# Performance work log

Hardware: AMD Instinct MI355X
Metric: run time of the kernel (lower is better)

The kernel has to match this reference:

```python
import jax, jax.numpy as jnp
import numpy as np

B, F, N, C = 2, 16, 128, 1280
MID = 128
CH = [320, 640, 1280, 1280]
DS = [16, 32, 64, 64]


def setup_inputs() -> dict:
    key = jax.random.key(0)
    ks = jax.random.split(key, 16)
    inp = {}
    inp["point_embedding"] = jax.random.normal(ks[0], (B, N, C), jnp.float32)
    inp["keypoints"] = jax.random.uniform(ks[1], (B, F, N, 2), dtype=jnp.float32)
    inp["subsets"] = jax.random.randint(ks[2], (B, F, N), -1, 2).astype(jnp.int32)
    inp["pose_latents"] = jax.random.normal(ks[3], (B, F, 4, 32, 32), jnp.float32)
    inp["w1s"] = jax.random.normal(ks[4], (4, C, MID), jnp.float32) * 0.02
    inp["b1s"] = jnp.zeros((4, MID), jnp.float32)
    for l, ch in enumerate(CH):
        inp[f"w2_{l}"] = jax.random.normal(ks[5 + l], (MID, ch), jnp.float32) * 0.02
        inp[f"b2_{l}"] = jnp.zeros((ch,), jnp.float32)
    inp["w"] = 512
    inp["h"] = 512
    return inp


def _nearest(x, h2, w2):
    # torch nn.Upsample(mode='nearest'): src = floor(dst * in/out)
    H, W = x.shape[-2], x.shape[-1]
    ih = (jnp.arange(h2) * H) // h2
    iw = (jnp.arange(w2) * W) // w2
    return x[:, ih][:, :, iw]


def _core(point_embedding, keypoints, subsets, w1s, b1s, w2s, b2s, w, h):
    Bb, Nn, Cc = point_embedding.shape
    Ff = keypoints.shape[1]
    H0, W0 = h // DS[0], w // DS[0]
    dt = point_embedding.dtype

    kx, ky = keypoints[..., 0], keypoints[..., 1]            # [B,F,N]
    valid = (jnp.minimum(kx, ky) >= 0) & (subsets != -1)
    px = jnp.clip(jnp.floor(kx * W0).astype(jnp.int32), 0, W0 - 1)
    py = jnp.clip(jnp.floor(ky * H0).astype(jnp.int32), 0, H0 - 1)
    bf = jnp.arange(Bb)[:, None, None] * Ff + jnp.arange(Ff)[None, :, None]
    flat = jnp.where(valid, (bf * H0 + py) * W0 + px, 0).reshape(-1)
    wts = valid.astype(dt).reshape(-1)

    # hit count per cell; level_count = max(hits, 1) matches torch's count-from-one logic
    hits = jnp.zeros(Bb * Ff * H0 * W0, dt).at[flat].add(wts)
    emb = jnp.broadcast_to(point_embedding[:, None], (Bb, Ff, Nn, Cc)).reshape(-1, Cc)
    sums = jnp.zeros((Bb * Ff * H0 * W0, Cc), dt).at[flat].add(emb * wts[:, None])
    grid = (sums / jnp.maximum(hits, 1.0)[:, None]).reshape(Bb, Ff, H0, W0, Cc)
    mask = (hits > 0).astype(dt).reshape(Bb, Ff, H0, W0)

    outs = []
    for l in range(4):
        h2, w2 = h // DS[l], w // DS[l]
        hid = jax.nn.silu(jnp.einsum('bfhwc,cm->bfhwm', grid, w1s[l]) + b1s[l])
        feat = jnp.einsum('bfhwm,mk->bfhwk', hid, w2s[l]) + b2s[l]
        feat = feat * mask[..., None]
        feat = feat.reshape(Bb * Ff, H0, W0, -1)
        if (h2, w2) != (H0, W0):
            # torch bilinear, align_corners=False (half-pixel), no antialias
            feat = jax.image.resize(feat, (Bb * Ff, h2, w2, feat.shape[-1]),
                                    method='bilinear', antialias=False)
        m = _nearest(mask.reshape(Bb * Ff, H0, W0), h2, w2)
        feat = feat * m[..., None]
        outs.append(feat.reshape(Bb, Ff, h2, w2, -1).transpose(0, 1, 4, 2, 3))
    loss_mask = jnp.ones((Bb, Ff, 4, H0, W0), dt)  # loss_type='global'
    return tuple(outs), loss_mask


def reference(point_embedding, keypoints, subsets, pose_latents, w1s, b1s,
              w2_0, b2_0, w2_1, b2_1, w2_2, b2_2, w2_3, b2_3, w, h):
    outs, loss_mask = _core(point_embedding, keypoints, subsets, w1s, b1s,
                            (w2_0, w2_1, w2_2, w2_3), (b2_0, b2_1, b2_2, b2_3), w, h)
    return (*outs, loss_mask)
```

## Files before the change

kernel.cpp:

```cpp
#include <hip/hip_runtime.h>
#include <cstdint>
#include <cstddef>

#define NPT 128
#define CC 1280
#define MID 128

typedef __attribute__((ext_vector_type(8))) short bf16x8;
typedef __attribute__((ext_vector_type(4))) float f32x4;

__device__ __forceinline__ unsigned short f2bf(float f) {
  unsigned u = __builtin_bit_cast(unsigned, f);
  u += 0x7FFFu + ((u >> 16) & 1u);
  return (unsigned short)(u >> 16);
}

struct KArgs {
  const float *w2_0, *w2_1, *w2_2, *w2_3;
  unsigned short *W2T0, *W2T1, *W2T2, *W2T3;
  const float* kp;
  const int* subsets;
  int* counts;
  int* plist;
  float* lossm;
  const float* pe;
  const float* w1s;
  const float* b1s;
  float* part;
  unsigned short* H;
  const float *b20, *b21, *b22, *b23;
  float *out0, *out1, *out2, *out3;
};

__device__ __forceinline__ void pe1_unit(const KArgs& a, int unit, int tid, char* smem) {
  unsigned short* Asl = (unsigned short*)smem;
  unsigned short* Bsl = (unsigned short*)(smem + 8192);
  int nt = unit & 7, mt = (unit >> 3) & 3, kz = unit >> 5;
  int n0 = nt * 64, m0 = mt * 64;
  int l = n0 >> 7, m0c = n0 & 127;
  const float* wbase = a.w1s + (size_t)l * CC * MID + m0c;
  int lane = tid & 63;
  int wave = tid >> 6;
  int lr = lane & 15, lk = lane >> 4;
  int choff = (wave & 1) * 32, spoff = (wave >> 1) * 32;
  f32x4 acc00 = {0.f, 0.f, 0.f, 0.f}, acc01 = acc00, acc10 = acc00, acc11 = acc00;
  for (int sub = 0; sub < 5; ++sub) {
    int kc0 = kz * 320 + sub * 64;
    __syncthreads();
    for (int u = tid; u < 512; u += 256) {
      int r = u >> 3, g = u & 7;
      const float* src = a.pe + (size_t)(m0 + r) * CC + kc0 + g * 8;
      float4 v0 = *reinterpret_cast<const float4*>(src);
      float4 v1 = *reinterpret_cast<const float4*>(src + 4);
      uint4 pk;
      pk.x = (unsigned)f2bf(v0.x) | ((unsigned)f2bf(v0.y) << 16);
      pk.y = (unsigned)f2bf(v0.z) | ((unsigned)f2bf(v0.w) << 16);
      pk.z = (unsigned)f2bf(v1.x) | ((unsigned)f2bf(v1.y) << 16);
      pk.w = (unsigned)f2bf(v1.z) | ((unsigned)f2bf(v1.w) << 16);
      *reinterpret_cast<uint4*>(&Asl[r * 64 + ((g ^ (r & 7)) << 3)]) = pk;
    }
    for (int u = tid; u < 512; u += 256) {
      int r = u & 63, gg = u >> 6;
      float vv[8];
#pragma unroll
      for (int j = 0; j < 8; ++j)
        vv[j] = wbase[(size_t)(kc0 + gg * 8 + j) * MID + r];
      uint4 pk;
      pk.x = (unsigned)f2bf(vv[0]) | ((unsigned)f2bf(vv[1]) << 16);
      pk.y = (unsigned)f2bf(vv[2]) | ((unsigned)f2bf(vv[3]) << 16);
      pk.z = (unsigned)f2bf(vv[4]) | ((unsigned)f2bf(vv[5]) << 16);
      pk.w = (unsigned)f2bf(vv[6]) | ((unsigned)f2bf(vv[7]) << 16);
      *reinterpret_cast<uint4*>(&Bsl[r * 64 + ((gg ^ (r & 7)) << 3)]) = pk;
    }
    __syncthreads();
#pragma unroll
    for (int kk = 0; kk < 64; kk += 32) {
      int gbase = (kk >> 3) + lk;
      int r0w = choff + lr, r1w = choff + 16 + lr;
      int r0a = spoff + lr, r1a = spoff + 16 + lr;
      bf16x8 wf0 = *reinterpret_cast<const bf16x8*>(&Bsl[r0w * 64 + ((gbase ^ (r0w & 7)) << 3)]);
      bf16x8 wf1 = *reinterpret_cast<const bf16x8*>(&Bsl[r1w * 64 + ((gbase ^ (r1w & 7)) << 3)]);
      bf16x8 af0 = *reinterpret_cast<const bf16x8*>(&Asl[r0a * 64 + ((gbase ^ (r0a & 7)) << 3)]);
      bf16x8 af1 = *reinterpret_cast<const bf16x8*>(&Asl[r1a * 64 + ((gbase ^ (r1a & 7)) << 3)]);
      acc00 = __builtin_amdgcn_mfma_f32_16x16x32_bf16(wf0, af0, acc00, 0, 0, 0);
      acc01 = __builtin_amdgcn_mfma_f32_16x16x32_bf16(wf0, af1, acc01, 0, 0, 0);
      acc10 = __builtin_amdgcn_mfma_f32_16x16x32_bf16(wf1, af0, acc10, 0, 0, 0);
      acc11 = __builtin_amdgcn_mfma_f32_16x16x32_bf16(wf1, af1, acc11, 0, 0, 0);
    }
  }
  float* pb = a.part + (size_t)kz * 131072;
#define PEPI(ACC, CI, SI)                                                      \
  {                                                                            \
    int spl = spoff + (SI) * 16 + lr;                                          \
    int chl = choff + (CI) * 16 + lk * 4;                                      \
    float4 v = make_float4(ACC[0], ACC[1], ACC[2], ACC[3]);                    \
    *reinterpret_cast<float4*>(&pb[(size_t)(m0 + spl) * 512 + n0 + chl]) = v;  \
  }
  PEPI(acc00, 0, 0)
  PEPI(acc01, 0, 1)
  PEPI(acc10, 1, 0)
  PEPI(acc11, 1, 1)
#undef PEPI
}

__device__ __forceinline__ void cheap_unit(const KArgs& a, int c, int tid, char* smem) {
  if (c < 32) {
    int bf = c;
    int* lcnt = (int*)smem;
    for (int i = tid; i < 1024; i += 256) lcnt[i] = 0;
    __syncthreads();
    if (tid < NPT) {
      int p = bf * NPT + tid;
      float kx = a.kp[2 * p], ky = a.kp[2 * p + 1];
      int sub = a.subsets[p];
      if (fminf(kx, ky) >= 0.f && sub != -1) {
        int px = (int)floorf(kx * 32.f);
        px = px < 0 ? 0 : (px > 31 ? 31 : px);
        int py = (int)floorf(ky * 32.f);
        py = py < 0 ? 0 : (py > 31 ? 31 : py);
        int cell = py * 32 + px;
        int slot = atomicAdd(&lcnt[cell], 1);
        if (slot < 32) a.plist[((size_t)bf * 1024 + cell) * 32 + slot] = tid;
      }
    }
    __syncthreads();
    for (int i = tid; i < 1024; i += 256) a.counts[bf * 1024 + i] = lcnt[i];
  } else if (c < 472) {
    float (*ts)[33] = (float(*)[33])smem;
    int local = c - 32;
    const float* w2;
    unsigned short* wt;
    int ch;
    if (local < 40) { w2 = a.w2_0; wt = a.W2T0; ch = 320; }
    else if (local < 120) { w2 = a.w2_1; wt = a.W2T1; ch = 640; local -= 40; }
    else if (local < 280) { w2 = a.w2_2; wt = a.W2T2; ch = 1280; local -= 120; }
    else { w2 = a.w2_3; wt = a.W2T3; ch = 1280; local -= 280; }
    int ctiles = ch >> 5;
    int mt = local / ctiles, ct = local % ctiles;
    int m0 = mt * 32, c0 = ct * 32;
    int i = tid >> 5, j = tid & 31;
#pragma unroll
    for (int r = 0; r < 4; ++r) {
      int m = r * 8 + i;
      ts[m][j] = w2[(size_t)(m0 + m) * ch + c0 + j];
    }
    __syncthreads();
#pragma unroll
    for (int r = 0; r < 4; ++r) {
      int cc = r * 8 + i;
      wt[(size_t)(c0 + cc) * 128 + m0 + j] = f2bf(ts[j][cc]);
    }
  } else {
    int idx = (c - 472) * 256 + tid;
    *reinterpret_cast<float4*>(a.lossm + (size_t)idx * 4) = make_float4(1.f, 1.f, 1.f, 1.f);
  }
}

__device__ __forceinline__ void hid_range(const KArgs& a, int base, int n, int tid,
                                          int* ccache, int* lst) {
  if (tid < n) ccache[tid] = a.counts[base + tid];
  __syncthreads();
  for (int q = 0; q < n; ++q) {
    int c = ccache[q];
    if (c == 0) continue;
    __syncthreads();
    int cell = base + q;
    int cu = c < 32 ? c : 32;
    if (tid < cu) lst[tid] = a.plist[(size_t)cell * 32 + tid];
    __syncthreads();
    int bat = cell >> 14;
    float invc = 1.f / (float)c;
    float sx = 0.f, sy = 0.f;
    for (int i = 0; i < cu; ++i) {
      const float2* rp = reinterpret_cast<const float2*>(
          a.part + (size_t)(bat * NPT + lst[i]) * 512);
      float2 v0 = rp[tid];
      float2 v1 = rp[65536 + tid];
      float2 v2 = rp[131072 + tid];
      float2 v3 = rp[196608 + tid];
      sx += v0.x + v1.x + v2.x + v3.x;
      sy += v0.y + v1.y + v2.y + v3.y;
    }
    float2 b = reinterpret_cast<const float2*>(a.b1s)[tid];
    float t0 = sx * invc + b.x;
    float t1 = sy * invc + b.y;
    t0 = t0 / (1.f + expf(-t0));
    t1 = t1 / (1.f + expf(-t1));
    int j0 = tid * 2;
    int l0 = j0 >> 7, m = j0 & 127;
    unsigned pk = (unsigned)f2bf(t0) | ((unsigned)f2bf(t1) << 16);
    *reinterpret_cast<unsigned*>(&a.H[(size_t)l0 * 4194304 + (size_t)cell * 128 + m]) = pk;
  }
}

template <int LOGW, int SCALE, int OFF, bool GATED>
__device__ __forceinline__ void mgemm_body(int bx, int byg,
                                           const unsigned short* __restrict__ Hl,
                                           const unsigned short* __restrict__ W2,
                                           const float* __restrict__ b2,
                                           const int* __restrict__ counts,
                                           float* __restrict__ out, int ch,
                                           unsigned short* Asl, unsigned short* Wsl,
                                           float* Ssl, float* Mnl) {
  const int W = 1 << LOGW;
  const int SDIM = 1 << (2 * LOGW);
  int r0 = bx * 64;
  int img = r0 >> (2 * LOGW);
  int tid = threadIdx.x;
  if (GATED) {
    for (int idx = tid; idx < 1024; idx += 256) {
      int r = idx >> 4, g = idx & 15;
      uint4 v = make_uint4(0u, 0u, 0u, 0u);
      if (counts[r0 + r] > 0)
        v = *reinterpret_cast<const uint4*>(Hl + (size_t)(r0 + r) * 128 + g * 8);
      *reinterpret_cast<uint4*>(&Asl[r * 128 + ((g ^ (r & 7)) << 3)]) = v;
    }
    if (tid < 64) {
      float mv = counts[r0 + tid] > 0 ? 1.f : 0.f;
      Ssl[tid] = mv;
      Mnl[tid] = mv;
    }
  } else {
    for (int idx = tid; idx < 1024; idx += 256) {
      int r = idx >> 4, g = idx & 15;
      int cr = r0 + r;
      int sp = cr & (SDIM - 1);
      int y = sp >> LOGW, x = sp & (W - 1);
      int c00 = (cr >> (2 * LOGW)) * 1024 + (SCALE * y + OFF) * 32 + (SCALE * x + OFF);
      int n00 = counts[c00], n01 = counts[c00 + 1];
      int n10 = counts[c00 + 32], n11 = counts[c00 + 33];
      float acc[8] = {};
#define ADDCELL(CELL)                                                      \
      {                                                                    \
        uint4 hv = *reinterpret_cast<const uint4*>(Hl + (size_t)(CELL) * 128 + g * 8); \
        unsigned uu[4] = {hv.x, hv.y, hv.z, hv.w};                         \
        _Pragma("unroll")                                                  \
        for (int qq = 0; qq < 4; ++qq) {                                   \
          acc[2 * qq] += __builtin_bit_cast(float, uu[qq] << 16);          \
          acc[2 * qq + 1] += __builtin_bit_cast(float, uu[qq] & 0xFFFF0000u); \
        }                                                                  \
      }
      if (n00 > 0) ADDCELL(c00)
      if (n01 > 0) ADDCELL(c00 + 1)
      if (n10 > 0) ADDCELL(c00 + 32)
      if (n11 > 0) ADDCELL(c00 + 33)
#undef ADDCELL
      unsigned short pk[8];
#pragma unroll
      for (int qq = 0; qq < 8; ++qq) pk[qq] = f2bf(0.25f * acc[qq]);
      uint4 v;
      v.x = (unsigned)pk[0] | ((unsigned)pk[1] << 16);
      v.y = (unsigned)pk[2] | ((unsigned)pk[3] << 16);
      v.z = (unsigned)pk[4] | ((unsigned)pk[5] << 16);
      v.w = (unsigned)pk[6] | ((unsigned)pk[7] << 16);
      *reinterpret_cast<uint4*>(&Asl[r * 128 + ((g ^ (r & 7)) << 3)]) = v;
    }
    if (tid < 64) {
      int cr = r0 + tid;
      int sp = cr & (SDIM - 1);
      int y = sp >> LOGW, x = sp & (W - 1);
      int ib = (cr >> (2 * LOGW)) * 1024;
      int c00 = ib + (SCALE * y + OFF) * 32 + (SCALE * x + OFF);
      float sm = (counts[c00] > 0 ? 1.f : 0.f) + (counts[c00 + 1] > 0 ? 1.f : 0.f) +
                 (counts[c00 + 32] > 0 ? 1.f : 0.f) + (counts[c00 + 33] > 0 ? 1.f : 0.f);
      Ssl[tid] = 0.25f * sm;
      Mnl[tid] = counts[ib + (SCALE * y) * 32 + SCALE * x] > 0 ? 1.f : 0.f;
    }
  }
  int lane = tid & 63;
  int wave = tid >> 6;
  int lr = lane & 15, lk = lane >> 4;
  int choff = (wave & 1) * 32, spoff = (wave >> 1) * 32;

  for (int it = 0; it < 5; ++it) {
    int k0 = (byg * 5 + it) * 64;
    __syncthreads();
    for (int idx = tid; idx < 1024; idx += 256) {
      int r = idx >> 4, g = idx & 15;
      uint4 v = *reinterpret_cast<const uint4*>(W2 + (size_t)(k0 + r) * 128 + g * 8);
      *reinterpret_cast<uint4*>(&Wsl[r * 128 + ((g ^ (r & 7)) << 3)]) = v;
    }
    __syncthreads();
    f32x4 a00 = {0.f, 0.f, 0.f, 0.f}, a01 = a00, a10 = a00, a11 = a00;
#pragma unroll
    for (int kk = 0; kk < 128; kk += 32) {
      int gbase = (kk >> 3) + lk;
      int r0w = choff + lr, r1w = choff + 16 + lr;
      int r0a = spoff + lr, r1a = spoff + 16 + lr;
      bf16x8 wf0 = *reinterpret_cast<const bf16x8*>(&Wsl[r0w * 128 + ((gbase ^ (r0w & 7)) << 3)]);
      bf16x8 wf1 = *reinterpret_cast<const bf16x8*>(&Wsl[r1w * 128 + ((gbase ^ (r1w & 7)) << 3)]);
      bf16x8 af0 = *reinterpret_cast<const bf16x8*>(&Asl[r0a * 128 + ((gbase ^ (r0a & 7)) << 3)]);
      bf16x8 af1 = *reinterpret_cast<const bf16x8*>(&Asl[r1a * 128 + ((gbase ^ (r1a & 7)) << 3)]);
      a00 = __builtin_amdgcn_mfma_f32_16x16x32_bf16(wf0, af0, a00, 0, 0, 0);
      a01 = __builtin_amdgcn_mfma_f32_16x16x32_bf16(wf0, af1, a01, 0, 0, 0);
      a10 = __builtin_amdgcn_mfma_f32_16x16x32_bf16(wf1, af0, a10, 0, 0, 0);
      a11 = __builtin_amdgcn_mfma_f32_16x16x32_bf16(wf1, af1, a11, 0, 0, 0);
    }
#define EPI(ACC, CI, SI)                                                          \
    {                                                                             \
      int spl = spoff + (SI) * 16 + lr;                                           \
      int absrow = r0 + spl;                                                      \
      float ss = Ssl[spl], mn = Mnl[spl];                                         \
      float* op = out + (size_t)img * ch * SDIM + (absrow & (SDIM - 1));          \
      _Pragma("unroll")                                                           \
      for (int rr = 0; rr < 4; ++rr) {                                            \
        int chl = k0 + choff + (CI) * 16 + lk * 4 + rr;                           \
        op[(size_t)chl * SDIM] = mn * (ACC[rr] + ss * b2[chl]);                   \
      }                                                                           \
    }
    EPI(a00, 0, 0)
    EPI(a01, 0, 1)
    EPI(a10, 1, 0)
    EPI(a11, 1, 1)
#undef EPI
  }
}

__device__ __forceinline__ void mgemm_unit(const KArgs& a, int unit, char* smem) {
  unsigned short* Asl = (unsigned short*)smem;
  unsigned short* Wsl = (unsigned short*)(smem + 16384);
  float* Ssl = (float*)(smem + 32768);
  float* Mnl = (float*)(smem + 33024);
  if (unit < 512) {
    mgemm_body<5, 1, 0, true>(unit, 0, a.H, a.W2T0, a.b20, a.counts, a.out0, 320,
                              Asl, Wsl, Ssl, Mnl);
  } else if (unit < 768) {
    int l = unit - 512;
    mgemm_body<4, 2, 0, false>(l & 127, l >> 7, a.H + 4194304, a.W2T1, a.b21, a.counts,
                               a.out1, 640, Asl, Wsl, Ssl, Mnl);
  } else if (unit < 896) {
    int l = unit - 768;
    mgemm_body<3, 4, 1, false>(l & 31, l >> 5, a.H + 2 * 4194304, a.W2T2, a.b22, a.counts,
                               a.out2, 1280, Asl, Wsl, Ssl, Mnl);
  } else {
    int l = unit - 896;
    mgemm_body<3, 4, 1, false>(l & 31, l >> 5, a.H + 3 * 4194304, a.W2T3, a.b23, a.counts,
                               a.out3, 1280, Asl, Wsl, Ssl, Mnl);
  }
}

__global__ __launch_bounds__(256) void k_preF(KArgs a) {
  __shared__ __align__(16) char smem[17408];
  int b = blockIdx.x;
  if (b < 128) pe1_unit(a, b, threadIdx.x, smem);
  else cheap_unit(a, b - 128, threadIdx.x, smem);
}
__global__ __launch_bounds__(256) void k_hidF(KArgs a) {
  __shared__ int ccache[8];
  __shared__ int lst[32];
  hid_range(a, blockIdx.x * 8, 8, threadIdx.x, ccache, lst);
}
__global__ __launch_bounds__(256) void k_mgemmF(KArgs a) {
  __shared__ __align__(16) char smem[33280];
  mgemm_unit(a, blockIdx.x, smem);
}

extern "C" void kernel_launch(void* const* d_in, const int* in_sizes, int n_in,
                              void* d_out, int out_size, void* d_ws, size_t ws_size,
                              hipStream_t stream) {
  float* out = (float*)d_out;

  float* part = (float*)d_ws;
  int* counts = (int*)(part + 524288);
  int* plist = counts + 32768;
  unsigned short* H = (unsigned short*)(plist + 1048576);
  unsigned short* W2T0 = H + 16777216;
  unsigned short* W2T1 = W2T0 + 40960;
  unsigned short* W2T2 = W2T1 + 81920;
  unsigned short* W2T3 = W2T2 + 163840;

  KArgs ka;
  ka.w2_0 = (const float*)d_in[6];
  ka.w2_1 = (const float*)d_in[8];
  ka.w2_2 = (const float*)d_in[10];
  ka.w2_3 = (const float*)d_in[12];
  ka.W2T0 = W2T0; ka.W2T1 = W2T1; ka.W2T2 = W2T2; ka.W2T3 = W2T3;
  ka.kp = (const float*)d_in[1];
  ka.subsets = (const int*)d_in[2];
  ka.counts = counts;
  ka.plist = plist;
  ka.lossm = out + 20971520;
  ka.pe = (const float*)d_in[0];
  ka.w1s = (const float*)d_in[4];
  ka.b1s = (const float*)d_in[5];
  ka.part = part;
  ka.H = H;
  ka.b20 = (const float*)d_in[7];
  ka.b21 = (const float*)d_in[9];
  ka.b22 = (const float*)d_in[11];
  ka.b23 = (const float*)d_in[13];
  ka.out0 = out;
  ka.out1 = out + 10485760;
  ka.out2 = out + 15728640;
  ka.out3 = out + 18350080;

  k_preF<<<dim3(728), dim3(256), 0, stream>>>(ka);
  k_hidF<<<dim3(4096), dim3(256), 0, stream>>>(ka);
  k_mgemmF<<<dim3(1024), dim3(256), 0, stream>>>(ka);
}
```

Measured before the change: 46.42 us.

## Fuse hidden-layer SiLU computation into mgemm A-tile load, drop k_hidF kernel

Removes the separate hidden-activation kernel and its bf16 H buffer. Each mgemm block now gathers per-point partial W1 products directly, averages them per cell, applies bias and SiLU, and builds its A tile in shared memory. This saves a kernel launch and an H write/read round trip. In exchange, hidden values are recomputed per channel-split block and per bilinear neighbour cell, which adds redundant global gathers and expf work on levels 1-3.

Result: faster. 45.06 us (-2.9%).

```diff
diff --git a/kernel.cpp b/kernel.cpp
--- a/kernel.cpp
+++ b/kernel.cpp
@@ -27,7 +27,6 @@
   const float* w1s;
   const float* b1s;
   float* part;
-  unsigned short* H;
   const float *b20, *b21, *b22, *b23;
   float *out0, *out1, *out2, *out3;
 };
@@ -156,49 +155,14 @@
   }
 }
 
-__device__ __forceinline__ void hid_range(const KArgs& a, int base, int n, int tid,
-                                          int* ccache, int* lst) {
-  if (tid < n) ccache[tid] = a.counts[base + tid];
-  __syncthreads();
-  for (int q = 0; q < n; ++q) {
-    int c = ccache[q];
-    if (c == 0) continue;
-    __syncthreads();
-    int cell = base + q;
-    int cu = c < 32 ? c : 32;
-    if (tid < cu) lst[tid] = a.plist[(size_t)cell * 32 + tid];
-    __syncthreads();
-    int bat = cell >> 14;
-    float invc = 1.f / (float)c;
-    float sx = 0.f, sy = 0.f;
-    for (int i = 0; i < cu; ++i) {
-      const float2* rp = reinterpret_cast<const float2*>(
-          a.part + (size_t)(bat * NPT + lst[i]) * 512);
-      float2 v0 = rp[tid];
-      float2 v1 = rp[65536 + tid];
-      float2 v2 = rp[131072 + tid];
-      float2 v3 = rp[196608 + tid];
-      sx += v0.x + v1.x + v2.x + v3.x;
-      sy += v0.y + v1.y + v2.y + v3.y;
-    }
-    float2 b = reinterpret_cast<const float2*>(a.b1s)[tid];
-    float t0 = sx * invc + b.x;
-    float t1 = sy * invc + b.y;
-    t0 = t0 / (1.f + expf(-t0));
-    t1 = t1 / (1.f + expf(-t1));
-    int j0 = tid * 2;
-    int l0 = j0 >> 7, m = j0 & 127;
-    unsigned pk = (unsigned)f2bf(t0) | ((unsigned)f2bf(t1) << 16);
-    *reinterpret_cast<unsigned*>(&a.H[(size_t)l0 * 4194304 + (size_t)cell * 128 + m]) = pk;
-  }
-}
-
 template <int LOGW, int SCALE, int OFF, bool GATED>
-__device__ __forceinline__ void mgemm_body(int bx, int byg,
-                                           const unsigned short* __restrict__ Hl,
+__device__ __forceinline__ void mgemm_body(int bx, int byg, int lvl,
+                                           const float* __restrict__ part,
+                                           const int* __restrict__ counts,
+                                           const int* __restrict__ plist,
+                                           const float* __restrict__ b1s,
                                            const unsigned short* __restrict__ W2,
                                            const float* __restrict__ b2,
-                                           const int* __restrict__ counts,
                                            float* __restrict__ out, int ch,
                                            unsigned short* Asl, unsigned short* Wsl,
                                            float* Ssl, float* Mnl) {
@@ -207,56 +171,68 @@
   int r0 = bx * 64;
   int img = r0 >> (2 * LOGW);
   int tid = threadIdx.x;
-  if (GATED) {
-    for (int idx = tid; idx < 1024; idx += 256) {
-      int r = idx >> 4, g = idx & 15;
-      uint4 v = make_uint4(0u, 0u, 0u, 0u);
-      if (counts[r0 + r] > 0)
-        v = *reinterpret_cast<const uint4*>(Hl + (size_t)(r0 + r) * 128 + g * 8);
-      *reinterpret_cast<uint4*>(&Asl[r * 128 + ((g ^ (r & 7)) << 3)]) = v;
-    }
-    if (tid < 64) {
-      float mv = counts[r0 + tid] > 0 ? 1.f : 0.f;
+
+  for (int idx = tid; idx < 1024; idx += 256) {
+    int r = idx >> 4, g = idx & 15;
+    int cr = r0 + r;
+    const float* b1p = b1s + lvl * 128 + g * 8;
+    float b1v[8];
+#pragma unroll
+    for (int j = 0; j < 8; ++j) b1v[j] = b1p[j];
+    int c00;
+    if (GATED) {
+      c00 = cr;
+    } else {
+      int sp = cr & (SDIM - 1);
+      int y = sp >> LOGW, x = sp & (W - 1);
+      c00 = (cr >> (2 * LOGW)) * 1024 + (SCALE * y + OFF) * 32 + (SCALE * x + OFF);
+    }
+    float a8[8] = {};
+#pragma unroll
+    for (int cc = 0; cc < (GATED ? 1 : 4); ++cc) {
+      int cell = c00 + (cc & 1) + (cc >> 1) * 32;
+      int cnt = counts[cell];
+      if (cnt > 0) {
+        int cu = cnt < 32 ? cnt : 32;
+        int bat = cell >> 14;
+        float c8[8] = {};
+        for (int i = 0; i < cu; ++i) {
+          int p = plist[(size_t)cell * 32 + i];
+          const float* rp = part + (size_t)(bat * NPT + p) * 512 + lvl * 128 + g * 8;
+#pragma unroll
+          for (int z = 0; z < 4; ++z) {
+            float4 v0 = *reinterpret_cast<const float4*>(rp + z * 131072);
+            float4 v1 = *reinterpret_cast<const float4*>(rp + z * 131072 + 4);
+            c8[0] += v0.x; c8[1] += v0.y; c8[2] += v0.z; c8[3] += v0.w;
+            c8[4] += v1.x; c8[5] += v1.y; c8[6] += v1.z; c8[7] += v1.w;
+          }
+        }
+        float invc = 1.f / (float)cnt;
+#pragma unroll
+        for (int j = 0; j < 8; ++j) {
+          float t = c8[j] * invc + b1v[j];
+          a8[j] += t / (1.f + expf(-t));
+        }
+      }
+    }
+    const float sc = GATED ? 1.f : 0.25f;
+    unsigned short pk[8];
+#pragma unroll
+    for (int j = 0; j < 8; ++j) pk[j] = f2bf(sc * a8[j]);
+    uint4 v;
+    v.x = (unsigned)pk[0] | ((unsigned)pk[1] << 16);
+    v.y = (unsigned)pk[2] | ((unsigned)pk[3] << 16);
+    v.z = (unsigned)pk[4] | ((unsigned)pk[5] << 16);
+    v.w = (unsigned)pk[6] | ((unsigned)pk[7] << 16);
+    *reinterpret_cast<uint4*>(&Asl[r * 128 + ((g ^ (r & 7)) << 3)]) = v;
+  }
+  if (tid < 64) {
+    int cr = r0 + tid;
+    if (GATED) {
+      float mv = counts[cr] > 0 ? 1.f : 0.f;
       Ssl[tid] = mv;
       Mnl[tid] = mv;
-    }
-  } else {
-    for (int idx = tid; idx < 1024; idx += 256) {
-      int r = idx >> 4, g = idx & 15;
-      int cr = r0 + r;
-      int sp = cr & (SDIM - 1);
-      int y = sp >> LOGW, x = sp & (W - 1);
-      int c00 = (cr >> (2 * LOGW)) * 1024 + (SCALE * y + OFF) * 32 + (SCALE * x + OFF);
-      int n00 = counts[c00], n01 = counts[c00 + 1];
-      int n10 = counts[c00 + 32], n11 = counts[c00 + 33];
-      float acc[8] = {};
-#define ADDCELL(CELL)                                                      \
-      {                                                                    \
-        uint4 hv = *reinterpret_cast<const uint4*>(Hl + (size_t)(CELL) * 128 + g * 8); \
-        unsigned uu[4] = {hv.x, hv.y, hv.z, hv.w};                         \
-        _Pragma("unroll")                                                  \
-        for (int qq = 0; qq < 4; ++qq) {                                   \
-          acc[2 * qq] += __builtin_bit_cast(float, uu[qq] << 16);          \
-          acc[2 * qq + 1] += __builtin_bit_cast(float, uu[qq] & 0xFFFF0000u); \
-        }                                                                  \
-      }
-      if (n00 > 0) ADDCELL(c00)
-      if (n01 > 0) ADDCELL(c00 + 1)
-      if (n10 > 0) ADDCELL(c00 + 32)
-      if (n11 > 0) ADDCELL(c00 + 33)
-#undef ADDCELL
-      unsigned short pk[8];
-#pragma unroll
-      for (int qq = 0; qq < 8; ++qq) pk[qq] = f2bf(0.25f * acc[qq]);
-      uint4 v;
-      v.x = (unsigned)pk[0] | ((unsigned)pk[1] << 16);
-      v.y = (unsigned)pk[2] | ((unsigned)pk[3] << 16);
-      v.z = (unsigned)pk[4] | ((unsigned)pk[5] << 16);
-      v.w = (unsigned)pk[6] | ((unsigned)pk[7] << 16);
-      *reinterpret_cast<uint4*>(&Asl[r * 128 + ((g ^ (r & 7)) << 3)]) = v;
-    }
-    if (tid < 64) {
-      int cr = r0 + tid;
+    } else {
       int sp = cr & (SDIM - 1);
       int y = sp >> LOGW, x = sp & (W - 1);
       int ib = (cr >> (2 * LOGW)) * 1024;
@@ -322,20 +298,20 @@
   float* Ssl = (float*)(smem + 32768);
   float* Mnl = (float*)(smem + 33024);
   if (unit < 512) {
-    mgemm_body<5, 1, 0, true>(unit, 0, a.H, a.W2T0, a.b20, a.counts, a.out0, 320,
-                              Asl, Wsl, Ssl, Mnl);
+    mgemm_body<5, 1, 0, true>(unit, 0, 0, a.part, a.counts, a.plist, a.b1s,
+                              a.W2T0, a.b20, a.out0, 320, Asl, Wsl, Ssl, Mnl);
   } else if (unit < 768) {
     int l = unit - 512;
-    mgemm_body<4, 2, 0, false>(l & 127, l >> 7, a.H + 4194304, a.W2T1, a.b21, a.counts,
-                               a.out1, 640, Asl, Wsl, Ssl, Mnl);
+    mgemm_body<4, 2, 0, false>(l & 127, l >> 7, 1, a.part, a.counts, a.plist, a.b1s,
+                               a.W2T1, a.b21, a.out1, 640, Asl, Wsl, Ssl, Mnl);
   } else if (unit < 896) {
     int l = unit - 768;
-    mgemm_body<3, 4, 1, false>(l & 31, l >> 5, a.H + 2 * 4194304, a.W2T2, a.b22, a.counts,
-                               a.out2, 1280, Asl, Wsl, Ssl, Mnl);
+    mgemm_body<3, 4, 1, false>(l & 31, l >> 5, 2, a.part, a.counts, a.plist, a.b1s,
+                               a.W2T2, a.b22, a.out2, 1280, Asl, Wsl, Ssl, Mnl);
   } else {
     int l = unit - 896;
-    mgemm_body<3, 4, 1, false>(l & 31, l >> 5, a.H + 3 * 4194304, a.W2T3, a.b23, a.counts,
-                               a.out3, 1280, Asl, Wsl, Ssl, Mnl);
+    mgemm_body<3, 4, 1, false>(l & 31, l >> 5, 3, a.part, a.counts, a.plist, a.b1s,
+                               a.W2T3, a.b23, a.out3, 1280, Asl, Wsl, Ssl, Mnl);
   }
 }
 
@@ -345,11 +321,6 @@
   if (b < 128) pe1_unit(a, b, threadIdx.x, smem);
   else cheap_unit(a, b - 128, threadIdx.x, smem);
 }
-__global__ __launch_bounds__(256) void k_hidF(KArgs a) {
-  __shared__ int ccache[8];
-  __shared__ int lst[32];
-  hid_range(a, blockIdx.x * 8, 8, threadIdx.x, ccache, lst);
-}
 __global__ __launch_bounds__(256) void k_mgemmF(KArgs a) {
   __shared__ __align__(16) char smem[33280];
   mgemm_unit(a, blockIdx.x, smem);
@@ -363,8 +334,7 @@
   float* part = (float*)d_ws;
   int* counts = (int*)(part + 524288);
   int* plist = counts + 32768;
-  unsigned short* H = (unsigned short*)(plist + 1048576);
-  unsigned short* W2T0 = H + 16777216;
+  unsigned short* W2T0 = (unsigned short*)(plist + 1048576);
   unsigned short* W2T1 = W2T0 + 40960;
   unsigned short* W2T2 = W2T1 + 81920;
   unsigned short* W2T3 = W2T2 + 163840;
@@ -384,7 +354,6 @@
   ka.w1s = (const float*)d_in[4];
   ka.b1s = (const float*)d_in[5];
   ka.part = part;
-  ka.H = H;
   ka.b20 = (const float*)d_in[7];
   ka.b21 = (const float*)d_in[9];
   ka.b22 = (const float*)d_in[11];
@@ -395,6 +364,5 @@
   ka.out3 = out + 18350080;
 
   k_preF<<<dim3(728), dim3(256), 0, stream>>>(ka);
-  k_hidF<<<dim3(4096), dim3(256), 0, stream>>>(ka);
   k_mgemmF<<<dim3(1024), dim3(256), 0, stream>>>(ka);
 }
```
